# Optimization experiments

Measured on AMD Instinct MI355X. Metric: run time of the kernel, lower is better.

Reference implementation:

```python
import jax, jax.numpy as jnp
import numpy as np

N = 100000   # nodes
E = 1600000  # edges


def setup_inputs() -> dict:
    key = jax.random.key(0)
    ks = jax.random.split(key, 9)
    return {
        "in_feat": jax.random.normal(ks[0], (N, 256), jnp.float32),
        "W": jax.random.normal(ks[1], (256, 128), jnp.float32) * 0.05,
        "attn_l": jax.random.normal(ks[2], (1, 128), jnp.float32) * 0.1,
        "attn_r": jax.random.normal(ks[3], (1, 128), jnp.float32) * 0.1,
        "bias": jax.random.normal(ks[4], (1, 128), jnp.float32) * 0.01,
        "fc_w": jax.random.normal(ks[5], (128, 2), jnp.float32) * 0.1,
        "fc_b": jax.random.normal(ks[6], (2,), jnp.float32) * 0.01,
        "src": jax.random.randint(ks[7], (E,), 0, N, jnp.int32),
        "dst": jax.random.randint(ks[8], (E,), 0, N, jnp.int32),
    }


def reference(in_feat, W, attn_l, attn_r, bias, fc_w, fc_b, src, dst):
    # GATConv, num_heads=1 (head dim kept implicit since it is squeezed anyway)
    h = in_feat @ W                              # [N, F] projected features
    el = jnp.sum(h * attn_l, axis=-1)            # [N] left attention logits
    er = jnp.sum(h * attn_r, axis=-1)            # [N] right attention logits
    e = jax.nn.leaky_relu(el[src] + er[dst], negative_slope=0.2)  # [E]
    # edge softmax segmented by destination node (numerically stable)
    m = jax.ops.segment_max(e, dst, num_segments=N)               # [N]
    ex = jnp.exp(e - m[dst])                                      # [E]
    s = jax.ops.segment_sum(ex, dst, num_segments=N)              # [N]
    alpha = ex / jnp.where(s == 0, 1.0, s)[dst]                   # [E]
    # attention-weighted aggregation of source features to destinations
    agg = jax.ops.segment_sum(alpha[:, None] * h[src], dst, num_segments=N)  # [N, F]
    agg = agg + bias                                              # GATConv bias
    # head: ReLU -> Linear -> sigmoid
    out = jax.nn.sigmoid(jax.nn.relu(agg) @ fc_w + fc_b)          # [N, C]
    return out
```

## Files before the change

kernel.cpp:

```cpp
#include <hip/hip_runtime.h>
#include <cstdint>
#include <cstddef>

#define N_NODES 100000
#define E_EDGES 1600000
#define F_IN 256
#define F_OUT 128
#define NBKT 391
#define OBCAP 5120
#define GEMM_NB 1563
#define WCVT_NB 128

#define GLOBAL_AS __attribute__((address_space(1)))
#define LDS_AS    __attribute__((address_space(3)))

typedef __attribute__((ext_vector_type(8))) short  short8v;
typedef __attribute__((ext_vector_type(4))) float  float4v;

__device__ __forceinline__ unsigned short f2bf(float x) {
    union { float f; unsigned u; } v; v.f = x;
    unsigned r = v.u + 0x7fffu + ((v.u >> 16) & 1u);
    return (unsigned short)(r >> 16);
}

__device__ __forceinline__ unsigned cvt_pk_bf16(float lo, float hi) {
    unsigned r;
    asm("v_cvt_pk_bf16_f32 %0, %1, %2" : "=v"(r) : "v"(lo), "v"(hi));
    return r;
}

__global__ __launch_bounds__(256) void wcvt_hist(const float* __restrict__ W,
                                                 unsigned short* __restrict__ Wt,
                                                 const int* __restrict__ dst,
                                                 int* __restrict__ bcnt) {
    __shared__ int h[NBKT];
    int t = threadIdx.x;
    if (blockIdx.x < WCVT_NB) {
        int i = blockIdx.x * 256 + t;
        int k = i >> 7, j = i & 127;
        Wt[j * F_IN + k] = f2bf(W[i]);
        return;
    }
    int b = blockIdx.x - WCVT_NB;
    for (int i = t; i < NBKT; i += 256) h[i] = 0;
    __syncthreads();
    int e0  = b * 4096;
    int end = min(e0 + 4096, E_EDGES);
    for (int i = e0 + t; i < end; i += 256) atomicAdd(&h[dst[i] >> 8], 1);
    __syncthreads();
    for (int i = t; i < NBKT; i += 256) if (h[i]) atomicAdd(&bcnt[i], h[i]);
}

__global__ __launch_bounds__(512) void k_scan(const int* __restrict__ bcnt,
                                              int* __restrict__ bbase,
                                              int* __restrict__ bcur) {
    __shared__ int s[512];
    int t = threadIdx.x;
    int d = (t < NBKT) ? bcnt[t] : 0;
    s[t] = d;
    __syncthreads();
    for (int off = 1; off < 512; off <<= 1) {
        int v = (t >= off) ? s[t - off] : 0;
        __syncthreads();
        s[t] += v;
        __syncthreads();
    }
    if (t < NBKT) { int ex = s[t] - d; bbase[t] = ex; bcur[t] = ex; }
    if (t == NBKT - 1) bbase[NBKT] = s[t];
}

__global__ __launch_bounds__(256) void gemm_scatter(const float* __restrict__ A,
                                                    const unsigned short* __restrict__ Wt,
                                                    const float* __restrict__ attn_l,
                                                    const float* __restrict__ attn_r,
                                                    unsigned short* __restrict__ Hb,
                                                    float* __restrict__ el,
                                                    float* __restrict__ er,
                                                    const int* __restrict__ src,
                                                    const int* __restrict__ dst,
                                                    int* __restrict__ bcur,
                                                    unsigned int* __restrict__ epack) {
    __shared__ char smem[32 * 1024];
    int tid = threadIdx.x;

    if (blockIdx.x >= GEMM_NB) {
        int* h = (int*)smem;
        int b = blockIdx.x - GEMM_NB;
        for (int i = tid; i < NBKT; i += 256) h[i] = 0;
        __syncthreads();
        int e0  = b * 4096;
        int end = min(e0 + 4096, E_EDGES);
        #pragma unroll
        for (int j = 0; j < 16; ++j) {
            int i = e0 + j * 256 + tid;
            if (i < end) atomicAdd(&h[dst[i] >> 8], 1);
        }
        __syncthreads();
        for (int i = tid; i < NBKT; i += 256) {
            int c = h[i];
            h[i] = c ? atomicAdd(&bcur[i], c) : 0;
        }
        __syncthreads();
        #pragma unroll
        for (int j = 0; j < 16; ++j) {
            int i = e0 + j * 256 + tid;
            if (i < end) {
                int dv = dst[i];
                int p = atomicAdd(&h[dv >> 8], 1);
                epack[p] = (unsigned)src[i] | ((unsigned)(dv & 255) << 17);
            }
        }
        return;
    }

    float*          Afs = (float*)smem;
    unsigned short* Bs  = (unsigned short*)(smem + 16 * 1024);
    int wave = tid >> 6, lane = tid & 63;
    int g = lane >> 4, c = lane & 15;
    int row0 = blockIdx.x * 64;
    float4v acc[8] = {};

    int a_r[4], a_k[4], a_w[4];
    #pragma unroll
    for (int i = 0; i < 4; ++i) {
        int W_ = i * 1024 + tid * 4;
        int r  = W_ >> 6;
        a_w[i] = W_;
        a_r[i] = min(row0 + r, N_NODES - 1);
        a_k[i] = (W_ & 63) ^ ((r & 15) << 2);
    }
    int b_j[4], b_k[4], b_u[4];
    #pragma unroll
    for (int i = 0; i < 4; ++i) {
        int U_ = i * 2048 + tid * 8;
        int j  = U_ >> 6;
        b_u[i] = U_;
        b_j[i] = j;
        b_k[i] = (U_ & 63) ^ ((j & 7) << 3);
    }

    for (int k0 = 0; k0 < F_IN; k0 += 64) {
        #pragma unroll
        for (int i = 0; i < 4; ++i) {
            __builtin_amdgcn_global_load_lds(
                (const GLOBAL_AS unsigned int*)(A + (size_t)a_r[i] * F_IN + k0 + a_k[i]),
                (LDS_AS unsigned int*)&Afs[a_w[i]], 16, 0, 0);
        }
        #pragma unroll
        for (int i = 0; i < 4; ++i) {
            __builtin_amdgcn_global_load_lds(
                (const GLOBAL_AS unsigned int*)(Wt + (size_t)b_j[i] * F_IN + k0 + b_k[i]),
                (LDS_AS unsigned int*)&Bs[b_u[i]], 16, 0, 0);
        }
        __syncthreads();
        int arow = wave * 16 + c;
        int aswz = (arow & 15) << 2;
        #pragma unroll
        for (int ks = 0; ks < 2; ++ks) {
            int woff = arow * 64 + ks * 32 + g * 8;
            float4 a0 = *reinterpret_cast<float4*>(&Afs[(woff)     ^ aswz]);
            float4 a1 = *reinterpret_cast<float4*>(&Afs[(woff + 4) ^ aswz]);
            unsigned u[4];
            u[0] = cvt_pk_bf16(a0.x, a0.y);
            u[1] = cvt_pk_bf16(a0.z, a0.w);
            u[2] = cvt_pk_bf16(a1.x, a1.y);
            u[3] = cvt_pk_bf16(a1.z, a1.w);
            short8v af = *reinterpret_cast<short8v*>(u);
            #pragma unroll
            for (int nt = 0; nt < 8; ++nt) {
                int j = nt * 16 + c;
                int boff = (j * 64 + ks * 32 + g * 8) ^ ((j & 7) << 3);
                short8v bf = *reinterpret_cast<short8v*>(&Bs[boff]);
                acc[nt] = __builtin_amdgcn_mfma_f32_16x16x32_bf16(af, bf, acc[nt], 0, 0, 0);
            }
        }
        __syncthreads();
    }

    float al[8], ar[8];
    #pragma unroll
    for (int nt = 0; nt < 8; ++nt) {
        al[nt] = attn_l[nt * 16 + c];
        ar[nt] = attn_r[nt * 16 + c];
    }
    #pragma unroll
    for (int r = 0; r < 4; ++r) {
        int grow = row0 + wave * 16 + g * 4 + r;
        float sl = 0.f, sr = 0.f;
        #pragma unroll
        for (int nt = 0; nt < 8; ++nt) {
            float h = acc[nt][r];
            sl += h * al[nt];
            sr += h * ar[nt];
        }
        if (grow < N_NODES) {
            #pragma unroll
            for (int nt = 0; nt < 8; ++nt)
                Hb[(size_t)grow * F_OUT + nt * 16 + c] = f2bf(acc[nt][r]);
        }
        #pragma unroll
        for (int off = 1; off < 16; off <<= 1) {
            sl += __shfl_xor(sl, off);
            sr += __shfl_xor(sr, off);
        }
        if (c == 0 && grow < N_NODES) { el[grow] = sl; er[grow] = sr; }
    }
}

__global__ __launch_bounds__(256) void k_sort2(const unsigned int* __restrict__ epack,
                                               const int* __restrict__ bbase,
                                               int* __restrict__ esrc,
                                               int* __restrict__ rowptr,
                                               int* __restrict__ deg) {
    __shared__ int hist[256], cur[256], s[256];
    __shared__ int obuf[OBCAP];
    int b = blockIdx.x, t = threadIdx.x;
    int base = bbase[b], end = bbase[b + 1];
    int cnt  = end - base;
    hist[t] = 0;
    __syncthreads();
    for (int i = t; i < cnt; i += 256) atomicAdd(&hist[epack[base + i] >> 17], 1);
    __syncthreads();
    int d = hist[t];
    s[t] = d;
    __syncthreads();
    for (int off = 1; off < 256; off <<= 1) {
        int v = (t >= off) ? s[t - off] : 0;
        __syncthreads();
        s[t] += v;
        __syncthreads();
    }
    int excl = s[t] - d;
    int n = b * 256 + t;
    if (n < N_NODES) { deg[n] = d; rowptr[n] = base + excl; }
    cur[t] = excl;
    __syncthreads();
    for (int i = t; i < cnt; i += 256) {
        unsigned e = epack[base + i];
        int p = atomicAdd(&cur[e >> 17], 1);
        if (p < OBCAP) obuf[p] = (int)(e & 0x1FFFFu);
    }
    __syncthreads();
    for (int i = t; i < cnt; i += 256) esrc[base + i] = obuf[i];
}

__global__ __launch_bounds__(256) void agg_fused(const int* __restrict__ rowptr,
                                                 const int* __restrict__ deg,
                                                 const int* __restrict__ esrc,
                                                 const float* __restrict__ el,
                                                 const float* __restrict__ er,
                                                 const char* __restrict__ Hc,
                                                 const float* __restrict__ bias,
                                                 const float* __restrict__ fcw,
                                                 const float* __restrict__ fcb,
                                                 float* __restrict__ out) {
    int tid  = threadIdx.x;
    int wid  = (blockIdx.x * 256 + tid) >> 6;
    int lane = tid & 63;
    if (wid >= N_NODES) return;
    int grp = lane >> 4, fl = lane & 15;
    int start = rowptr[wid];
    int dg    = deg[wid];
    float ern = er[wid];
    float exsum = 0.f;
    float acc[8] = {};
    unsigned flb = (unsigned)fl << 4;

    #pragma unroll 2
    for (int q = grp; q < dg; q += 4) {
        int sid = esrc[start + q];
        float tv = el[(unsigned)sid] + ern;
        tv = tv > 0.f ? tv : 0.2f * tv;
        float ex = __expf(tv);
        exsum += ex;
        uint4 v = *(const uint4*)(Hc + (((unsigned)sid << 8) + flb));
        acc[0] += ex * __uint_as_float(v.x << 16);
        acc[1] += ex * __uint_as_float(v.x & 0xffff0000u);
        acc[2] += ex * __uint_as_float(v.y << 16);
        acc[3] += ex * __uint_as_float(v.y & 0xffff0000u);
        acc[4] += ex * __uint_as_float(v.z << 16);
        acc[5] += ex * __uint_as_float(v.z & 0xffff0000u);
        acc[6] += ex * __uint_as_float(v.w << 16);
        acc[7] += ex * __uint_as_float(v.w & 0xffff0000u);
    }

    float ssum = exsum;
    ssum += __shfl_xor(ssum, 16);
    ssum += __shfl_xor(ssum, 32);
    #pragma unroll
    for (int j = 0; j < 8; ++j) {
        acc[j] += __shfl_xor(acc[j], 16);
        acc[j] += __shfl_xor(acc[j], 32);
    }
    float scale = ssum > 0.f ? 1.f / ssum : 0.f;

    float4 b0 = ((const float4*)bias)[fl * 2];
    float4 b1 = ((const float4*)bias)[fl * 2 + 1];
    float d0 = 0.f, d1 = 0.f;
    #pragma unroll
    for (int j = 0; j < 8; ++j) {
        float bj = j < 4 ? (&b0.x)[j] : (&b1.x)[j - 4];
        float vv = fmaxf(acc[j] * scale + bj, 0.f);
        float2 wj = ((const float2*)fcw)[fl * 8 + j];
        d0 += vv * wj.x;
        d1 += vv * wj.y;
    }
    #pragma unroll
    for (int off = 1; off < 16; off <<= 1) {
        d0 += __shfl_xor(d0, off);
        d1 += __shfl_xor(d1, off);
    }
    if (lane == 0) {
        out[(size_t)wid * 2 + 0] = 1.f / (1.f + __expf(-(d0 + fcb[0])));
        out[(size_t)wid * 2 + 1] = 1.f / (1.f + __expf(-(d1 + fcb[1])));
    }
}

extern "C" void kernel_launch(void* const* d_in, const int* in_sizes, int n_in,
                              void* d_out, int out_size, void* d_ws, size_t ws_size,
                              hipStream_t stream) {
    const float* in_feat = (const float*)d_in[0];
    const float* W       = (const float*)d_in[1];
    const float* attn_l  = (const float*)d_in[2];
    const float* attn_r  = (const float*)d_in[3];
    const float* bias    = (const float*)d_in[4];
    const float* fc_w    = (const float*)d_in[5];
    const float* fc_b    = (const float*)d_in[6];
    const int*   src     = (const int*)d_in[7];
    const int*   dst     = (const int*)d_in[8];
    float* out = (float*)d_out;

    char* p = (char*)d_ws;
    unsigned short* HB = (unsigned short*)p; p += (size_t)N_NODES * F_OUT * sizeof(unsigned short);
    unsigned short* WT = (unsigned short*)p; p += (size_t)F_IN * F_OUT * sizeof(unsigned short);
    float* EL     = (float*)p; p += (size_t)N_NODES * sizeof(float);
    float* ER     = (float*)p; p += (size_t)N_NODES * sizeof(float);
    int*   DEG    = (int*)p;   p += (size_t)N_NODES * sizeof(int);
    int*   ROWPTR = (int*)p;   p += (size_t)N_NODES * sizeof(int);
    int*   BCNT   = (int*)p;   p += 512 * sizeof(int);
    int*   BBASE  = (int*)p;   p += 512 * sizeof(int);
    int*   BCUR   = (int*)p;   p += 512 * sizeof(int);
    unsigned int* EPACK = (unsigned int*)p; p += (size_t)E_EDGES * sizeof(unsigned int);
    int*   ESRC   = (int*)p;   p += (size_t)E_EDGES * sizeof(int);

    hipMemsetAsync(BCNT, 0, 512 * sizeof(int), stream);

    wcvt_hist<<<WCVT_NB + NBKT, 256, 0, stream>>>(W, WT, dst, BCNT);
    k_scan   <<<1, 512, 0, stream>>>(BCNT, BBASE, BCUR);
    gemm_scatter<<<GEMM_NB + NBKT, 256, 0, stream>>>(
        in_feat, WT, attn_l, attn_r, HB, EL, ER, src, dst, BCUR, EPACK);
    k_sort2  <<<NBKT, 256, 0, stream>>>(EPACK, BBASE, ESRC, ROWPTR, DEG);

    agg_fused<<<(N_NODES * 64 + 255) / 256, 256, 0, stream>>>(
        ROWPTR, DEG, ESRC, EL, ER, (const char*)HB, bias, fc_w, fc_b, out);
}
```

Before: 150.2 us.

## Compute normalized edge attention in sort kernel and stage it through LDS

The per-edge logit, exp and segment sum move from the aggregation kernel into the bucket-sort kernel, which now writes pre-normalized alpha plus a pre-shifted source byte offset as a float2 per edge. The aggregation wave loads 64 edge records coalesced into LDS and broadcasts them to its four lane groups, dropping the random el gather and the exp from the hot loop. The cost is doubled per-edge storage (8 bytes instead of 4), larger LDS use and float atomics in the sort kernel. Like the original, it skips max subtraction, so very large logits could overflow.

```diff
diff --git a/kernel.cpp b/kernel.cpp
--- a/kernel.cpp
+++ b/kernel.cpp
@@ -209,15 +209,20 @@
 
 __global__ __launch_bounds__(256) void k_sort2(const unsigned int* __restrict__ epack,
                                                const int* __restrict__ bbase,
-                                               int* __restrict__ esrc,
+                                               const float* __restrict__ el,
+                                               const float* __restrict__ er,
+                                               float2* __restrict__ exs,
                                                int* __restrict__ rowptr,
                                                int* __restrict__ deg) {
     __shared__ int hist[256], cur[256], s[256];
-    __shared__ int obuf[OBCAP];
+    __shared__ float ssl[256];
+    __shared__ unsigned obuf[OBCAP];
+    __shared__ float exb[OBCAP];
     int b = blockIdx.x, t = threadIdx.x;
     int base = bbase[b], end = bbase[b + 1];
     int cnt  = end - base;
     hist[t] = 0;
+    ssl[t] = 0.f;
     __syncthreads();
     for (int i = t; i < cnt; i += 256) atomicAdd(&hist[epack[base + i] >> 17], 1);
     __syncthreads();
@@ -237,62 +242,73 @@
     __syncthreads();
     for (int i = t; i < cnt; i += 256) {
         unsigned e = epack[base + i];
-        int p = atomicAdd(&cur[e >> 17], 1);
-        if (p < OBCAP) obuf[p] = (int)(e & 0x1FFFFu);
-    }
-    __syncthreads();
-    for (int i = t; i < cnt; i += 256) esrc[base + i] = obuf[i];
+        int d2  = e >> 17;
+        int sid = (int)(e & 0x1FFFFu);
+        float tv = el[sid] + er[b * 256 + d2];
+        tv = tv > 0.f ? tv : 0.2f * tv;
+        float ex = __expf(tv);
+        int p = atomicAdd(&cur[d2], 1);
+        if (p < OBCAP) { obuf[p] = e; exb[p] = ex; }
+        atomicAdd(&ssl[d2], ex);
+    }
+    __syncthreads();
+    for (int i = t; i < cnt; i += 256) {
+        unsigned e = obuf[i];
+        float alpha = exb[i] / ssl[e >> 17];
+        exs[base + i] = make_float2(alpha, __uint_as_float((e & 0x1FFFFu) << 8));
+    }
 }
 
 __global__ __launch_bounds__(256) void agg_fused(const int* __restrict__ rowptr,
                                                  const int* __restrict__ deg,
-                                                 const int* __restrict__ esrc,
-                                                 const float* __restrict__ el,
-                                                 const float* __restrict__ er,
+                                                 const float2* __restrict__ exs,
                                                  const char* __restrict__ Hc,
                                                  const float* __restrict__ bias,
                                                  const float* __restrict__ fcw,
                                                  const float* __restrict__ fcb,
                                                  float* __restrict__ out) {
-    int tid  = threadIdx.x;
-    int wid  = (blockIdx.x * 256 + tid) >> 6;
-    int lane = tid & 63;
+    __shared__ float2 exbuf[4][64];
+    int tid   = threadIdx.x;
+    int wslot = tid >> 6;
+    int wid   = (blockIdx.x * 256 + tid) >> 6;
+    int lane  = tid & 63;
     if (wid >= N_NODES) return;
     int grp = lane >> 4, fl = lane & 15;
     int start = rowptr[wid];
     int dg    = deg[wid];
-    float ern = er[wid];
-    float exsum = 0.f;
     float acc[8] = {};
+    float2* eb = exbuf[wslot];
     unsigned flb = (unsigned)fl << 4;
 
-    #pragma unroll 2
-    for (int q = grp; q < dg; q += 4) {
-        int sid = esrc[start + q];
-        float tv = el[(unsigned)sid] + ern;
-        tv = tv > 0.f ? tv : 0.2f * tv;
-        float ex = __expf(tv);
-        exsum += ex;
-        uint4 v = *(const uint4*)(Hc + (((unsigned)sid << 8) + flb));
-        acc[0] += ex * __uint_as_float(v.x << 16);
-        acc[1] += ex * __uint_as_float(v.x & 0xffff0000u);
-        acc[2] += ex * __uint_as_float(v.y << 16);
-        acc[3] += ex * __uint_as_float(v.y & 0xffff0000u);
-        acc[4] += ex * __uint_as_float(v.z << 16);
-        acc[5] += ex * __uint_as_float(v.z & 0xffff0000u);
-        acc[6] += ex * __uint_as_float(v.w << 16);
-        acc[7] += ex * __uint_as_float(v.w & 0xffff0000u);
-    }
-
-    float ssum = exsum;
-    ssum += __shfl_xor(ssum, 16);
-    ssum += __shfl_xor(ssum, 32);
+    for (int base = 0; base < dg; base += 64) {
+        int cnt = min(64, dg - base);
+        float2 p2 = make_float2(0.f, 0.f);
+        if (lane < cnt) p2 = exs[start + base + lane];
+        eb[lane] = p2;
+        __builtin_amdgcn_wave_barrier();
+        int nq = (cnt + 3) >> 2;
+        #pragma unroll 2
+        for (int q = 0; q < nq; ++q) {
+            float2 p = eb[q * 4 + grp];
+            float aq = p.x;
+            uint4 v = *(const uint4*)(Hc + (__float_as_uint(p.y) + flb));
+            acc[0] += aq * __uint_as_float(v.x << 16);
+            acc[1] += aq * __uint_as_float(v.x & 0xffff0000u);
+            acc[2] += aq * __uint_as_float(v.y << 16);
+            acc[3] += aq * __uint_as_float(v.y & 0xffff0000u);
+            acc[4] += aq * __uint_as_float(v.z << 16);
+            acc[5] += aq * __uint_as_float(v.z & 0xffff0000u);
+            acc[6] += aq * __uint_as_float(v.w << 16);
+            acc[7] += aq * __uint_as_float(v.w & 0xffff0000u);
+        }
+        __builtin_amdgcn_wave_barrier();
+    }
+
     #pragma unroll
     for (int j = 0; j < 8; ++j) {
         acc[j] += __shfl_xor(acc[j], 16);
         acc[j] += __shfl_xor(acc[j], 32);
     }
-    float scale = ssum > 0.f ? 1.f / ssum : 0.f;
 
     float4 b0 = ((const float4*)bias)[fl * 2];
     float4 b1 = ((const float4*)bias)[fl * 2 + 1];
@@ -300,7 +316,7 @@
     #pragma unroll
     for (int j = 0; j < 8; ++j) {
         float bj = j < 4 ? (&b0.x)[j] : (&b1.x)[j - 4];
-        float vv = fmaxf(acc[j] * scale + bj, 0.f);
+        float vv = fmaxf(acc[j] + bj, 0.f);
         float2 wj = ((const float2*)fcw)[fl * 8 + j];
         d0 += vv * wj.x;
         d1 += vv * wj.y;
@@ -341,7 +357,7 @@
     int*   BBASE  = (int*)p;   p += 512 * sizeof(int);
     int*   BCUR   = (int*)p;   p += 512 * sizeof(int);
     unsigned int* EPACK = (unsigned int*)p; p += (size_t)E_EDGES * sizeof(unsigned int);
-    int*   ESRC   = (int*)p;   p += (size_t)E_EDGES * sizeof(int);
+    float2* EXS   = (float2*)p; p += (size_t)E_EDGES * sizeof(float2);
 
     hipMemsetAsync(BCNT, 0, 512 * sizeof(int), stream);
 
@@ -349,8 +365,8 @@
     k_scan   <<<1, 512, 0, stream>>>(BCNT, BBASE, BCUR);
     gemm_scatter<<<GEMM_NB + NBKT, 256, 0, stream>>>(
         in_feat, WT, attn_l, attn_r, HB, EL, ER, src, dst, BCUR, EPACK);
-    k_sort2  <<<NBKT, 256, 0, stream>>>(EPACK, BBASE, ESRC, ROWPTR, DEG);
+    k_sort2  <<<NBKT, 256, 0, stream>>>(EPACK, BBASE, EL, ER, EXS, ROWPTR, DEG);
 
     agg_fused<<<(N_NODES * 64 + 255) / 256, 256, 0, stream>>>(
-        ROWPTR, DEG, ESRC, EL, ER, (const char*)HB, bias, fc_w, fc_b, out);
-}
+        ROWPTR, DEG, EXS, (const char*)HB, bias, fc_w, fc_b, out);
+}
```

Result: no change. 149.5 us (-0.5%).
